# Performance work log

Hardware: AMD Instinct MI355X
Metric: run time of the kernel (lower is better)

Reference implementation:

```python
import jax, jax.numpy as jnp
import numpy as np

G, N, EPG = 32, 128, 2048   # graphs, nodes/graph (uniform), edges/graph
H, L = 128, 2               # hidden_dim, num_layers
OUT = 12


def setup_inputs() -> dict:
    key = jax.random.key(0)
    ks = jax.random.split(key, 32)
    x = jax.random.randint(ks[0], (G * N, 9), 0, 2, dtype=jnp.int32)
    edge_attr = jax.random.randint(ks[1], (G * EPG, 3), 0, 2, dtype=jnp.int32)
    # edges stay within their own graph (global ids = local + graph offset)
    src = jax.random.randint(ks[2], (G, EPG), 0, N, dtype=jnp.int32)
    dst = jax.random.randint(ks[3], (G, EPG), 0, N, dtype=jnp.int32)
    off = (jnp.arange(G, dtype=jnp.int32) * N)[:, None]
    edge_index = jnp.stack([(src + off).reshape(-1), (dst + off).reshape(-1)]).astype(jnp.int64)
    batch_idx = (jnp.arange(G * N) // N).astype(jnp.int32)

    def p(k, shape, scale=0.05):
        return jax.random.normal(k, shape, dtype=jnp.float32) * scale

    return dict(
        x=x, edge_index=edge_index, edge_attr=edge_attr, batch_idx=batch_idx,
        atom_tab=p(ks[4], (9, 119, H)), bond_tab=p(ks[5], (3, 8, H)),
        W_m1=p(ks[6], (L, 2 * H, H)), b_m1=jnp.zeros((L, H), jnp.float32),
        W_m2=p(ks[7], (L, 2 * H, H)), b_m2=jnp.zeros((L, H), jnp.float32),
        W_me=p(ks[8], (L, H, H)), b_me=jnp.zeros((L, H), jnp.float32),
        W_mg=p(ks[9], (L, H, H)), b_mg=jnp.zeros((L, H), jnp.float32),
        W_h1=p(ks[10], (L, H, H)), b_h1=jnp.zeros((L, H), jnp.float32),
        W_h2=p(ks[11], (L, H, H)), b_h2=jnp.zeros((L, H), jnp.float32),
        W_o1=p(ks[12], (L, 2 * H, H)), b_o1=jnp.zeros((L, H), jnp.float32),
        W_o2=p(ks[13], (L, H, H)), b_o2=jnp.zeros((L, H), jnp.float32),
        Wg1=p(ks[14], (H, H)), bg1=jnp.zeros((H,), jnp.float32),
        Wg2=p(ks[15], (H, OUT)), bg2=jnp.zeros((OUT,), jnp.float32),
    )


def reference(x, edge_index, edge_attr, batch_idx, atom_tab, bond_tab,
              W_m1, b_m1, W_m2, b_m2, W_me, b_me, W_mg, b_mg,
              W_h1, b_h1, W_h2, b_h2, W_o1, b_o1, W_o2, b_o2,
              Wg1, bg1, Wg2, bg2):
    # Atom/Bond encoders: sum of per-feature embeddings
    node_fts = jnp.sum(jax.vmap(lambda t, i: t[i], in_axes=(0, 1))(atom_tab, x), axis=0)        # (G*N, H)
    edge_fts = jnp.sum(jax.vmap(lambda t, i: t[i], in_axes=(0, 1))(bond_tab, edge_attr), axis=0)  # (E, H)

    # dense adjacency + dense edge features (one fused scatter, replaces per-graph loop)
    g = (edge_index[0] // N).astype(jnp.int32)
    s = (edge_index[0] % N).astype(jnp.int32)
    d = (edge_index[1] % N).astype(jnp.int32)
    adj = jnp.zeros((G, N, N), jnp.float32).at[g, s, d].set(1.0)
    edense = jnp.zeros((G, N, N, H), jnp.float32).at[g, s, d].set(edge_fts)

    nd = node_fts.reshape(G, N, H)          # to_dense_batch (uniform graphs -> no padding)
    gf = jnp.zeros((G, H), jnp.float32)
    hid = jnp.zeros_like(nd)
    NEG = jnp.float32(-1e9)

    for l in range(L):  # CLRS MPNN layers
        z = jnp.concatenate([nd, hid], axis=-1)                 # (G, N, 2H)
        m1 = z @ W_m1[l] + b_m1[l]
        m2 = z @ W_m2[l] + b_m2[l]
        me = edense @ W_me[l] + b_me[l]                         # (G, N, N, H)
        mg = gf @ W_mg[l] + b_mg[l]
        msgs = m1[:, None, :, :] + m2[:, :, None, :] + me + mg[:, None, None, :]
        h = jax.nn.relu(msgs)
        h = jax.nn.relu(h @ W_h1[l] + b_h1[l]) @ W_h2[l] + b_h2[l]
        h = jnp.where(adj[..., None] > 0, h, NEG)               # masked max over senders
        agg = jnp.max(h, axis=1)                                # (G, N, H)
        hid = jax.nn.relu(z @ W_o1[l] + b_o1[l] + agg @ W_o2[l] + b_o2[l])

    emb = hid.mean(axis=1)                                      # (G, H)
    return jax.nn.relu(emb @ Wg1 + bg1) @ Wg2 + bg2             # (G, OUT)
```

## Files before the change

kernel.cpp:

```cpp
#include <hip/hip_runtime.h>

#define Gg   32
#define Nn   128
#define Hh   128
#define Ee   65536
#define GN   4096
#define GNN  524288

typedef unsigned short ushort_t;
typedef __attribute__((ext_vector_type(8))) __bf16 bf16x8;
typedef __attribute__((ext_vector_type(4))) float f32x4;
struct us4 { ushort_t a, b, c, d; };

__device__ __forceinline__ float reluf(float x) { return x > 0.f ? x : 0.f; }

__device__ __forceinline__ unsigned fkey(float f) {
  unsigned u = __float_as_uint(f);
  return (u & 0x80000000u) ? ~u : (u | 0x80000000u);
}
__device__ __forceinline__ float funkey(unsigned k) {
  unsigned u = (k & 0x80000000u) ? (k ^ 0x80000000u) : ~k;
  return __uint_as_float(u);
}

__device__ __forceinline__ ushort_t bfh(float x) {
  unsigned u = __float_as_uint(x);
  return (ushort_t)((u + 0x7FFFu + ((u >> 16) & 1u)) >> 16);
}
__device__ __forceinline__ void split2(float x, ushort_t& h, ushort_t& l) {
  h = bfh(x);
  float hf = __uint_as_float(((unsigned)h) << 16);
  l = bfh(x - hf);
}

__global__ __launch_bounds__(256) void k_wprep_all(const float* __restrict__ W_h1,
                                                   const float* __restrict__ W_h2,
                                                   const float* __restrict__ W_o1,
                                                   const float* __restrict__ W_o2,
                                                   const float* __restrict__ W_m1,
                                                   const float* __restrict__ W_m2,
                                                   ushort_t* __restrict__ wt,
                                                   ushort_t* __restrict__ wo,
                                                   ushort_t* __restrict__ wm,
                                                   int* __restrict__ win,
                                                   int* __restrict__ cnt) {
  int b = blockIdx.x;
  int tid = threadIdx.x;
  if (b < 256) {
    int t = b * 256 + tid;
    int l = t >> 15;
    int m = (t >> 14) & 1;
    int e = t & 16383;
    int n = e & 127, k = e >> 7;
    const float* W = (m == 0 ? W_h1 : W_h2) + l * 16384;
    float v = W[k * 128 + n];
    ushort_t h, lo;
    split2(v, h, lo);
    int nf = n >> 4, lr = n & 15, kf = k >> 5, lg = (k >> 3) & 3, j = k & 7;
    int off = ((nf * 4 + kf) * 64 + lg * 16 + lr) * 8 + j;
    int base = ((l * 2 + m) * 2) * 16384;
    wt[base + off] = h;
    wt[base + 16384 + off] = lo;
  } else if (b < 640) {
    int ep = (b - 256) * 256 + tid;
    int l = (ep >= 49152) ? 1 : 0;
    int e = ep - l * 49152;
    int n = e / 384, k = e - n * 384;
    float v = (k < 256) ? W_o1[(l * 256 + k) * 128 + n]
                        : W_o2[(l * 128 + (k - 256)) * 128 + n];
    ushort_t h, lo;
    split2(v, h, lo);
    int nf = n >> 4, lr = n & 15, kf = k >> 5, lg = (k >> 3) & 3, j = k & 7;
    int off = ((nf * 12 + kf) * 64 + lg * 16 + lr) * 8 + j;
    wo[(l * 2 + 0) * 49152 + off] = h;
    wo[(l * 2 + 1) * 49152 + off] = lo;
  } else if (b < 1152) {
    int t = (b - 640) * 256 + tid;
    int l = t >> 16;
    int m = (t >> 15) & 1;
    int e = t & 32767;
    int n = e >> 8, k = e & 255;
    const float* W = (m == 0 ? W_m1 : W_m2);
    float v = W[(l * 256 + k) * 128 + n];
    ushort_t h, lo;
    split2(v, h, lo);
    int nf = n >> 4, lr = n & 15, kf = k >> 5, lg = (k >> 3) & 3, j = k & 7;
    int off = ((nf * 8 + kf) * 64 + lg * 16 + lr) * 8 + j;
    int base = ((l * 2 + m) * 2) * 32768;
    wm[base + off] = h;
    wm[base + 32768 + off] = lo;
  } else {
    int idx = (b - 1152) * 256 + tid;
    ((int4*)win)[idx] = make_int4(-1, -1, -1, -1);
    if (idx == 0) *cnt = 0;
  }
}

__global__ __launch_bounds__(256) void k_scatter_win(const int* __restrict__ e32,
                                                     int* __restrict__ win) {
  __shared__ int sflag;
  int tid = threadIdx.x;
  if (tid == 0) sflag = 0;
  __syncthreads();
  if (tid < 128 && e32[2 * tid + 1] != 0) atomicOr(&sflag, 1);
  __syncthreads();
  int e = blockIdx.x * 256 + tid;
  int sg, dg;
  if (sflag) { sg = e32[e]; dg = e32[Ee + e]; }
  else       { sg = e32[2 * e]; dg = e32[2 * Ee + 2 * e]; }
  int g = sg / Nn;
  int s = sg % Nn;
  int d = dg % Nn;
  atomicMax(&win[(g * Nn + d) * Nn + s], e);
}

__global__ __launch_bounds__(256) void k_dfill2(const int* __restrict__ win,
                                                const int* __restrict__ eattr,
                                                int* __restrict__ cnt,
                                                unsigned* __restrict__ recs) {
  int tid = threadIdx.x;
  int grp = tid >> 7, t = tid & 127;
  int dest = blockIdx.x * 2 + grp;
  int e = win[dest * 128 + t];
  bool valid = e >= 0;
  unsigned long long mask = __ballot(valid);
  __shared__ int cw[4];
  __shared__ int sbase;
  int lane = tid & 63, wv = tid >> 6;
  if (lane == 0) cw[wv] = __popcll(mask);
  __syncthreads();
  if (tid == 0) {
    int tot = cw[0] + cw[1] + cw[2] + cw[3];
    sbase = tot ? atomicAdd(cnt, tot) : 0;
  }
  __syncthreads();
  if (valid) {
    int off = __popcll(mask & ((1ull << lane) - 1));
    if (wv & 1) off += cw[grp * 2];
    if (grp) off += cw[0] + cw[1];
    int a0 = eattr[e * 3 + 0], a1 = eattr[e * 3 + 1], a2 = eattr[e * 3 + 2];
    unsigned code = (unsigned)(a0 + (a1 << 3) + (a2 << 6));
    unsigned idx = ((unsigned)dest << 7) | (unsigned)t;
    recs[sbase + off] = (idx << 9) | code;
  }
}

__global__ __launch_bounds__(256) void k_me2(const float* __restrict__ bond_tab,
                                             const float* __restrict__ W_me,
                                             const float* __restrict__ b_me,
                                             const float* __restrict__ b_mg,
                                             float* __restrict__ me0,
                                             float* __restrict__ me1,
                                             unsigned* __restrict__ aggkA,
                                             unsigned* __restrict__ aggkB) {
  int bx = blockIdx.x;
  int l = bx >> 8, b2 = bx & 255;
  const float* W = W_me + l * 16384;
  const float* bme = b_me + l * 128;
  const float* bmg = b_mg + l * 128;
  float* me = l ? me1 : me0;
  unsigned* aggk = l ? aggkB : aggkA;
  __shared__ float v[2][128];
  int tid = threadIdx.x;
  int half = tid >> 7, j = tid & 127;
  int c = b2 * 2 + half;
  int a0 = c & 7, a1 = (c >> 3) & 7, a2 = (c >> 6) & 7;
  v[half][j] = bond_tab[a0 * 128 + j] + bond_tab[(8 + a1) * 128 + j] +
               bond_tab[(16 + a2) * 128 + j];
  __syncthreads();
  float acc = bme[j] + bmg[j];
  for (int i = 0; i < 128; ++i) acc += v[half][i] * W[i * 128 + j];
  me[c * 128 + j] = acc;
  unsigned key = fkey(-1.0e9f);
#pragma unroll
  for (int i = 0; i < 8; ++i) aggk[b2 * 2048 + i * 256 + tid] = key;
}

__device__ __forceinline__ void load_afrag(const ushort_t (*MH)[136],
                                           const ushort_t (*ML)[136],
                                           int row, int lg,
                                           bf16x8 ah[4], bf16x8 al[4]) {
#pragma unroll
  for (int kf = 0; kf < 4; ++kf) {
    ah[kf] = *(const bf16x8*)&MH[row][lg * 8 + 32 * kf];
    al[kf] = *(const bf16x8*)&ML[row][lg * 8 + 32 * kf];
  }
}

__device__ __forceinline__ void load_afrag264(const ushort_t (*MH)[264],
                                              const ushort_t (*ML)[264],
                                              int row, int base, int lg,
                                              bf16x8 ah[4], bf16x8 al[4]) {
#pragma unroll
  for (int kf = 0; kf < 4; ++kf) {
    ah[kf] = *(const bf16x8*)&MH[row][base + lg * 8 + 32 * kf];
    al[kf] = *(const bf16x8*)&ML[row][base + lg * 8 + 32 * kf];
  }
}

__global__ __launch_bounds__(256) void k_encode_m12(const int* __restrict__ x,
                                                    const float* __restrict__ atom_tab,
                                                    const ushort_t* __restrict__ wm,
                                                    const float* __restrict__ bi1,
                                                    const float* __restrict__ bi2,
                                                    float* __restrict__ nf_,
                                                    float* __restrict__ hid,
                                                    float* __restrict__ m1,
                                                    float* __restrict__ m2) {
  __shared__ ushort_t AH[16][136];
  __shared__ ushort_t AL[16][136];
  __shared__ int xs[144];
  int tid = threadIdx.x;
  int v0 = blockIdx.x * 16;
  if (tid < 144) xs[tid] = x[v0 * 9 + tid];
  __syncthreads();
#pragma unroll
  for (int i = 0; i < 8; ++i) {
    int e = tid + i * 256;
    int row = e >> 7, col = e & 127;
    float s = 0.f;
#pragma unroll
    for (int f = 0; f < 9; ++f) {
      int idx = xs[row * 9 + f];
      s += atom_tab[(f * 119 + idx) * Hh + col];
    }
    nf_[(v0 + row) * Hh + col] = s;
    hid[(v0 + row) * Hh + col] = 0.f;
    ushort_t h, l;
    split2(s, h, l);
    AH[row][col] = h;
    AL[row][col] = l;
  }
  __syncthreads();
  int lane = tid & 63, wid = tid >> 6;
  int lr = lane & 15, lg = lane >> 4;
  f32x4 a1[2], a2[2];
#pragma unroll
  for (int i = 0; i < 2; ++i) { a1[i] = (f32x4){0.f,0.f,0.f,0.f}; a2[i] = (f32x4){0.f,0.f,0.f,0.f}; }
  const ushort_t* w1h = wm;
  const ushort_t* w1l = wm + 32768;
  const ushort_t* w2h = wm + 65536;
  const ushort_t* w2l = wm + 98304;
  bf16x8 ah[4], al[4];
  load_afrag(AH, AL, lr, lg, ah, al);
#pragma unroll
  for (int jj = 0; jj < 2; ++jj) {
    int nfr = 2 * wid + jj;
#pragma unroll
    for (int kf = 0; kf < 4; ++kf) {
      int ch = ((nfr * 8 + kf) << 9) + lane * 8;
      bf16x8 b1h = *(const bf16x8*)(w1h + ch);
      bf16x8 b1l = *(const bf16x8*)(w1l + ch);
      bf16x8 b2h = *(const bf16x8*)(w2h + ch);
      bf16x8 b2l = *(const bf16x8*)(w2l + ch);
      a1[jj] = __builtin_amdgcn_mfma_f32_16x16x32_bf16(ah[kf], b1h, a1[jj], 0, 0, 0);
      a1[jj] = __builtin_amdgcn_mfma_f32_16x16x32_bf16(ah[kf], b1l, a1[jj], 0, 0, 0);
      a1[jj] = __builtin_amdgcn_mfma_f32_16x16x32_bf16(al[kf], b1h, a1[jj], 0, 0, 0);
      a2[jj] = __builtin_amdgcn_mfma_f32_16x16x32_bf16(ah[kf], b2h, a2[jj], 0, 0, 0);
      a2[jj] = __builtin_amdgcn_mfma_f32_16x16x32_bf16(ah[kf], b2l, a2[jj], 0, 0, 0);
      a2[jj] = __builtin_amdgcn_mfma_f32_16x16x32_bf16(al[kf], b2h, a2[jj], 0, 0, 0);
    }
  }
#pragma unroll
  for (int jj = 0; jj < 2; ++jj) {
    int col = 16 * (2 * wid + jj) + lr;
    float bb1 = bi1[col], bb2 = bi2[col];
#pragma unroll
    for (int reg = 0; reg < 4; ++reg) {
      int row = v0 + lg * 4 + reg;
      m1[row * Hh + col] = a1[jj][reg] + bb1;
      m2[row * Hh + col] = a2[jj][reg] + bb2;
    }
  }
}

__global__ __launch_bounds__(512) void k_edge(const unsigned* __restrict__ recs,
                                              const int* __restrict__ cnt,
                                              const float* __restrict__ m1,
                                              const float* __restrict__ m2,
                                              const float* __restrict__ me,
                                              const ushort_t* __restrict__ wt1h,
                                              const ushort_t* __restrict__ wt1l,
                                              const ushort_t* __restrict__ wt2h,
                                              const ushort_t* __restrict__ wt2l,
                                              const float* __restrict__ b_h1,
                                              const float* __restrict__ b_h2,
                                              unsigned* __restrict__ aggk) {
  __shared__ ushort_t MH[64][136];
  __shared__ ushort_t ML[64][136];
  __shared__ unsigned srec[64];
  int tid = threadIdx.x;
  int n = *cnt;
  if (tid < 64) {
    int r = blockIdx.x * 64 + tid;
    srec[tid] = (r < n) ? recs[r] : 0xFFFFFFFFu;
  }
  __syncthreads();
  {
    int c4 = tid & 31, rq = tid >> 5;
#pragma unroll
    for (int i = 0; i < 4; ++i) {
      int r = 16 * i + rq;
      float4 v = make_float4(0.f, 0.f, 0.f, 0.f);
      unsigned rec = srec[r];
      if (rec != 0xFFFFFFFFu) {
        int code = rec & 511;
        unsigned idx = rec >> 9;
        int s = idx & 127, d = (idx >> 7) & 127, g = idx >> 14;
        float4 a = *(const float4*)(m1 + (((g << 7) + d) << 7) + c4 * 4);
        float4 b = *(const float4*)(m2 + (((g << 7) + s) << 7) + c4 * 4);
        float4 cme = *(const float4*)(me + (code << 7) + c4 * 4);
        v.x = reluf(a.x + b.x + cme.x);
        v.y = reluf(a.y + b.y + cme.y);
        v.z = reluf(a.z + b.z + cme.z);
        v.w = reluf(a.w + b.w + cme.w);
      }
      us4 h4, l4;
      split2(v.x, h4.a, l4.a); split2(v.y, h4.b, l4.b);
      split2(v.z, h4.c, l4.c); split2(v.w, h4.d, l4.d);
      *(us4*)&MH[r][c4 * 4] = h4;
      *(us4*)&ML[r][c4 * 4] = l4;
    }
  }
  __syncthreads();

  int lane = tid & 63, wid = tid >> 6;
  int lr = lane & 15, lg = lane >> 4;
  float b1v = b_h1[16 * wid + lr];
  float b2v = b_h2[16 * wid + lr];
  f32x4 acc[4];
#pragma unroll
  for (int rg = 0; rg < 4; ++rg) acc[rg] = (f32x4){0.f, 0.f, 0.f, 0.f};
#pragma unroll
  for (int rg = 0; rg < 4; ++rg) {
    bf16x8 ah[4], al[4];
    load_afrag(MH, ML, 16 * rg + lr, lg, ah, al);
#pragma unroll
    for (int kf = 0; kf < 4; ++kf) {
      int ch = ((wid * 4 + kf) << 9) + lane * 8;
      bf16x8 bh = *(const bf16x8*)(wt1h + ch);
      bf16x8 bl = *(const bf16x8*)(wt1l + ch);
      acc[rg] = __builtin_amdgcn_mfma_f32_16x16x32_bf16(ah[kf], bh, acc[rg], 0, 0, 0);
      acc[rg] = __builtin_amdgcn_mfma_f32_16x16x32_bf16(ah[kf], bl, acc[rg], 0, 0, 0);
      acc[rg] = __builtin_amdgcn_mfma_f32_16x16x32_bf16(al[kf], bh, acc[rg], 0, 0, 0);
    }
  }
  __syncthreads();
#pragma unroll
  for (int rg = 0; rg < 4; ++rg)
#pragma unroll
    for (int reg = 0; reg < 4; ++reg) {
      float t = reluf(acc[rg][reg] + b1v);
      int row = 16 * rg + lg * 4 + reg;
      int col = 16 * wid + lr;
      ushort_t h, l;
      split2(t, h, l);
      MH[row][col] = h;
      ML[row][col] = l;
    }
  __syncthreads();
#pragma unroll
  for (int rg = 0; rg < 4; ++rg) acc[rg] = (f32x4){0.f, 0.f, 0.f, 0.f};
#pragma unroll
  for (int rg = 0; rg < 4; ++rg) {
    bf16x8 ah[4], al[4];
    load_afrag(MH, ML, 16 * rg + lr, lg, ah, al);
#pragma unroll
    for (int kf = 0; kf < 4; ++kf) {
      int ch = ((wid * 4 + kf) << 9) + lane * 8;
      bf16x8 bh = *(const bf16x8*)(wt2h + ch);
      bf16x8 bl = *(const bf16x8*)(wt2l + ch);
      acc[rg] = __builtin_amdgcn_mfma_f32_16x16x32_bf16(ah[kf], bh, acc[rg], 0, 0, 0);
      acc[rg] = __builtin_amdgcn_mfma_f32_16x16x32_bf16(ah[kf], bl, acc[rg], 0, 0, 0);
      acc[rg] = __builtin_amdgcn_mfma_f32_16x16x32_bf16(al[kf], bh, acc[rg], 0, 0, 0);
    }
  }
  __syncthreads();
#pragma unroll
  for (int rg = 0; rg < 4; ++rg)
#pragma unroll
    for (int reg = 0; reg < 4; ++reg) {
      int row = 16 * rg + lg * 4 + reg;
      int col = 16 * wid + lr;
      unsigned b = __float_as_uint(acc[rg][reg] + b2v);
      MH[row][col] = (ushort_t)(b >> 16);
      ML[row][col] = (ushort_t)(b & 0xFFFFu);
    }
  __syncthreads();
  {
    int c = tid & 127, quarter = tid >> 7;
    int rbeg = quarter * 16, rend = rbeg + 16;
    unsigned curkey = 0xFFFFu;
    float best = -3.0e38f;
    for (int r = rbeg; r < rend; ++r) {
      unsigned rec = srec[r];
      unsigned key = rec >> 16;
      if (key != curkey) {
        if (curkey != 0xFFFFu)
          atomicMax(aggk + (curkey << 7) + c, fkey(best));
        curkey = key;
        best = -3.0e38f;
      }
      if (key != 0xFFFFu) {
        unsigned b = ((unsigned)MH[r][c] << 16) | (unsigned)ML[r][c];
        best = fmaxf(best, __uint_as_float(b));
      }
    }
    if (curkey != 0xFFFFu)
      atomicMax(aggk + (curkey << 7) + c, fkey(best));
  }
}

__global__ __launch_bounds__(256) void k_out(const float* __restrict__ nf,
                                             const float* __restrict__ hid,
                                             const unsigned* __restrict__ aggk,
                                             const ushort_t* __restrict__ wo_h,
                                             const ushort_t* __restrict__ wo_l,
                                             const float* __restrict__ bo1,
                                             const float* __restrict__ bo2,
                                             float* __restrict__ hidn) {
  __shared__ ushort_t MH[16][136];
  __shared__ ushort_t ML[16][136];
  int tid = threadIdx.x;
  int v0 = blockIdx.x * 16;
  int lane = tid & 63, wid = tid >> 6;
  int lr = lane & 15, lg = lane >> 4;
  f32x4 acc[2];
#pragma unroll
  for (int jj = 0; jj < 2; ++jj) acc[jj] = (f32x4){0.f, 0.f, 0.f, 0.f};

  for (int seg = 0; seg < 3; ++seg) {
#pragma unroll
    for (int i = 0; i < 2; ++i) {
      int idx = tid + i * 256;
      int row = idx >> 5, c4 = idx & 31;
      float4 v;
      if (seg == 0)      v = ((const float4*)nf)[(v0 + row) * 32 + c4];
      else if (seg == 1) v = ((const float4*)hid)[(v0 + row) * 32 + c4];
      else {
        uint4 k4 = ((const uint4*)aggk)[(v0 + row) * 32 + c4];
        v.x = funkey(k4.x); v.y = funkey(k4.y); v.z = funkey(k4.z); v.w = funkey(k4.w);
      }
      us4 h4, l4;
      split2(v.x, h4.a, l4.a);
      split2(v.y, h4.b, l4.b);
      split2(v.z, h4.c, l4.c);
      split2(v.w, h4.d, l4.d);
      *(us4*)&MH[row][c4 * 4] = h4;
      *(us4*)&ML[row][c4 * 4] = l4;
    }
    __syncthreads();
    bf16x8 ah[4], al[4];
    load_afrag(MH, ML, lr, lg, ah, al);
#pragma unroll
    for (int jj = 0; jj < 2; ++jj) {
      int nfr = 2 * wid + jj;
#pragma unroll
      for (int kf = 0; kf < 4; ++kf) {
        int ch = ((nfr * 12 + seg * 4 + kf) << 9) + lane * 8;
        bf16x8 bh = *(const bf16x8*)(wo_h + ch);
        bf16x8 bl = *(const bf16x8*)(wo_l + ch);
        acc[jj] = __builtin_amdgcn_mfma_f32_16x16x32_bf16(ah[kf], bh, acc[jj], 0, 0, 0);
        acc[jj] = __builtin_amdgcn_mfma_f32_16x16x32_bf16(ah[kf], bl, acc[jj], 0, 0, 0);
        acc[jj] = __builtin_amdgcn_mfma_f32_16x16x32_bf16(al[kf], bh, acc[jj], 0, 0, 0);
      }
    }
    __syncthreads();
  }
#pragma unroll
  for (int jj = 0; jj < 2; ++jj) {
    int col = 16 * (2 * wid + jj) + lr;
    float b = bo1[col] + bo2[col];
#pragma unroll
    for (int reg = 0; reg < 4; ++reg)
      hidn[(v0 + lg * 4 + reg) * Hh + col] = reluf(acc[jj][reg] + b);
  }
}

__global__ __launch_bounds__(256) void k_out_m12(const float* __restrict__ nf,
                                                 const float* __restrict__ hid,
                                                 const unsigned* __restrict__ aggk,
                                                 const ushort_t* __restrict__ wo_h,
                                                 const ushort_t* __restrict__ wo_l,
                                                 const float* __restrict__ bo1,
                                                 const float* __restrict__ bo2,
                                                 const ushort_t* __restrict__ wm,
                                                 const float* __restrict__ bm1,
                                                 const float* __restrict__ bm2,
                                                 float* __restrict__ hidn,
                                                 float* __restrict__ m1,
                                                 float* __restrict__ m2) {
  __shared__ ushort_t AH[16][264];
  __shared__ ushort_t AL[16][264];
  int tid = threadIdx.x;
  int v0 = blockIdx.x * 16;
  int lane = tid & 63, wid = tid >> 6;
  int lr = lane & 15, lg = lane >> 4;
  f32x4 acc[2];
#pragma unroll
  for (int jj = 0; jj < 2; ++jj) acc[jj] = (f32x4){0.f, 0.f, 0.f, 0.f};

  for (int seg = 0; seg < 3; ++seg) {
#pragma unroll
    for (int i = 0; i < 2; ++i) {
      int idx = tid + i * 256;
      int row = idx >> 5, c4 = idx & 31;
      float4 v;
      if (seg == 0)      v = ((const float4*)nf)[(v0 + row) * 32 + c4];
      else if (seg == 1) v = ((const float4*)hid)[(v0 + row) * 32 + c4];
      else {
        uint4 k4 = ((const uint4*)aggk)[(v0 + row) * 32 + c4];
        v.x = funkey(k4.x); v.y = funkey(k4.y); v.z = funkey(k4.z); v.w = funkey(k4.w);
      }
      us4 h4, l4;
      split2(v.x, h4.a, l4.a);
      split2(v.y, h4.b, l4.b);
      split2(v.z, h4.c, l4.c);
      split2(v.w, h4.d, l4.d);
      *(us4*)&AH[row][c4 * 4] = h4;
      *(us4*)&AL[row][c4 * 4] = l4;
    }
    __syncthreads();
    bf16x8 ah[4], al[4];
    load_afrag264(AH, AL, lr, 0, lg, ah, al);
#pragma unroll
    for (int jj = 0; jj < 2; ++jj) {
      int nfr = 2 * wid + jj;
#pragma unroll
      for (int kf = 0; kf < 4; ++kf) {
        int ch = ((nfr * 12 + seg * 4 + kf) << 9) + lane * 8;
        bf16x8 bh = *(const bf16x8*)(wo_h + ch);
        bf16x8 bl = *(const bf16x8*)(wo_l + ch);
        acc[jj] = __builtin_amdgcn_mfma_f32_16x16x32_bf16(ah[kf], bh, acc[jj], 0, 0, 0);
        acc[jj] = __builtin_amdgcn_mfma_f32_16x16x32_bf16(ah[kf], bl, acc[jj], 0, 0, 0);
        acc[jj] = __builtin_amdgcn_mfma_f32_16x16x32_bf16(al[kf], bh, acc[jj], 0, 0, 0);
      }
    }
    __syncthreads();
  }
#pragma unroll
  for (int jj = 0; jj < 2; ++jj) {
    int col = 16 * (2 * wid + jj) + lr;
    float b = bo1[col] + bo2[col];
#pragma unroll
    for (int reg = 0; reg < 4; ++reg) {
      float hv = reluf(acc[jj][reg] + b);
      int row = lg * 4 + reg;
      hidn[(v0 + row) * Hh + col] = hv;
      ushort_t h, l;
      split2(hv, h, l);
      AH[row][128 + col] = h;
      AL[row][128 + col] = l;
    }
  }
#pragma unroll
  for (int i = 0; i < 2; ++i) {
    int idx = tid + i * 256;
    int row = idx >> 5, c4 = idx & 31;
    float4 v = ((const float4*)nf)[(v0 + row) * 32 + c4];
    us4 h4, l4;
    split2(v.x, h4.a, l4.a);
    split2(v.y, h4.b, l4.b);
    split2(v.z, h4.c, l4.c);
    split2(v.w, h4.d, l4.d);
    *(us4*)&AH[row][c4 * 4] = h4;
    *(us4*)&AL[row][c4 * 4] = l4;
  }
  __syncthreads();
  f32x4 a1[2], a2[2];
#pragma unroll
  for (int i = 0; i < 2; ++i) { a1[i] = (f32x4){0.f,0.f,0.f,0.f}; a2[i] = (f32x4){0.f,0.f,0.f,0.f}; }
  const ushort_t* w1h = wm;
  const ushort_t* w1l = wm + 32768;
  const ushort_t* w2h = wm + 65536;
  const ushort_t* w2l = wm + 98304;
#pragma unroll
  for (int seg = 0; seg < 2; ++seg) {
    bf16x8 ah[4], al[4];
    load_afrag264(AH, AL, lr, seg * 128, lg, ah, al);
#pragma unroll
    for (int jj = 0; jj < 2; ++jj) {
      int nfr = 2 * wid + jj;
#pragma unroll
      for (int kf = 0; kf < 4; ++kf) {
        int ch = ((nfr * 8 + seg * 4 + kf) << 9) + lane * 8;
        bf16x8 b1h = *(const bf16x8*)(w1h + ch);
        bf16x8 b1l = *(const bf16x8*)(w1l + ch);
        bf16x8 b2h = *(const bf16x8*)(w2h + ch);
        bf16x8 b2l = *(const bf16x8*)(w2l + ch);
        a1[jj] = __builtin_amdgcn_mfma_f32_16x16x32_bf16(ah[kf], b1h, a1[jj], 0, 0, 0);
        a1[jj] = __builtin_amdgcn_mfma_f32_16x16x32_bf16(ah[kf], b1l, a1[jj], 0, 0, 0);
        a1[jj] = __builtin_amdgcn_mfma_f32_16x16x32_bf16(al[kf], b1h, a1[jj], 0, 0, 0);
        a2[jj] = __builtin_amdgcn_mfma_f32_16x16x32_bf16(ah[kf], b2h, a2[jj], 0, 0, 0);
        a2[jj] = __builtin_amdgcn_mfma_f32_16x16x32_bf16(ah[kf], b2l, a2[jj], 0, 0, 0);
        a2[jj] = __builtin_amdgcn_mfma_f32_16x16x32_bf16(al[kf], b2h, a2[jj], 0, 0, 0);
      }
    }
  }
#pragma unroll
  for (int jj = 0; jj < 2; ++jj) {
    int col = 16 * (2 * wid + jj) + lr;
    float bb1 = bm1[col], bb2 = bm2[col];
#pragma unroll
    for (int reg = 0; reg < 4; ++reg) {
      int row = v0 + lg * 4 + reg;
      m1[row * Hh + col] = a1[jj][reg] + bb1;
      m2[row * Hh + col] = a2[jj][reg] + bb2;
    }
  }
}

__global__ __launch_bounds__(128) void k_head(const float* __restrict__ hid,
                                              const float* __restrict__ Wg1,
                                              const float* __restrict__ bg1,
                                              const float* __restrict__ Wg2,
                                              const float* __restrict__ bg2,
                                              float* __restrict__ out) {
  __shared__ float emb[Hh];
  __shared__ float tt[Hh];
  int g = blockIdx.x, j = threadIdx.x;
  float s = 0.f;
  for (int n = 0; n < Nn; ++n) s += hid[(g * Nn + n) * Hh + j];
  emb[j] = s * (1.f / Nn);
  __syncthreads();
  float a = bg1[j];
  for (int i = 0; i < Hh; ++i) a += emb[i] * Wg1[i * Hh + j];
  tt[j] = reluf(a);
  __syncthreads();
  if (j < 12) {
    float o = bg2[j];
    for (int i = 0; i < Hh; ++i) o += tt[i] * Wg2[i * 12 + j];
    out[g * 12 + j] = o;
  }
}

extern "C" void kernel_launch(void* const* d_in, const int* in_sizes, int n_in,
                              void* d_out, int out_size, void* d_ws, size_t ws_size,
                              hipStream_t stream) {
  const int* x = (const int*)d_in[0];
  const int* eidx32 = (const int*)d_in[1];
  const int* eattr = (const int*)d_in[2];
  const float* atom_tab = (const float*)d_in[4];
  const float* bond_tab = (const float*)d_in[5];
  const float* W_m1 = (const float*)d_in[6];
  const float* b_m1 = (const float*)d_in[7];
  const float* W_m2 = (const float*)d_in[8];
  const float* b_m2 = (const float*)d_in[9];
  const float* W_me = (const float*)d_in[10];
  const float* b_me = (const float*)d_in[11];
  const float* b_mg = (const float*)d_in[13];
  const float* W_h1 = (const float*)d_in[14];
  const float* b_h1 = (const float*)d_in[15];
  const float* W_h2 = (const float*)d_in[16];
  const float* b_h2 = (const float*)d_in[17];
  const float* W_o1 = (const float*)d_in[18];
  const float* b_o1 = (const float*)d_in[19];
  const float* W_o2 = (const float*)d_in[20];
  const float* b_o2 = (const float*)d_in[21];
  const float* Wg1 = (const float*)d_in[22];
  const float* bg1 = (const float*)d_in[23];
  const float* Wg2 = (const float*)d_in[24];
  const float* bg2 = (const float*)d_in[25];
  float* out = (float*)d_out;

  char* ws = (char*)d_ws;
  float* nf = (float*)(ws);
  float* hidA = (float*)(ws + (2u << 20));
  float* hidB = (float*)(ws + (4u << 20));
  float* m1 = (float*)(ws + (6u << 20));
  float* m2 = (float*)(ws + (8u << 20));
  unsigned* aggkA = (unsigned*)(ws + (10u << 20));
  int* win = (int*)(ws + (12u << 20));
  ushort_t* wt = (ushort_t*)(ws + (14u << 20));
  float* me0 = (float*)(ws + (14u << 20) + (256u << 10));
  float* me1 = (float*)(ws + (14u << 20) + (512u << 10));
  unsigned* recs = (unsigned*)(ws + (15u << 20));
  int* cnt = (int*)(ws + (15u << 20) + (256u << 10));
  unsigned* aggkB = (unsigned*)(ws + (16u << 20));
  ushort_t* wo = (ushort_t*)(ws + (18u << 20));
  ushort_t* wm = (ushort_t*)(ws + (18u << 20) + (512u << 10));

  k_wprep_all<<<1664, 256, 0, stream>>>(W_h1, W_h2, W_o1, W_o2, W_m1, W_m2,
                                        wt, wo, wm, win, cnt);
  k_me2<<<512, 256, 0, stream>>>(bond_tab, W_me, b_me, b_mg, me0, me1, aggkA, aggkB);
  k_encode_m12<<<256, 256, 0, stream>>>(x, atom_tab, wm, b_m1, b_m2,
                                        nf, hidA, m1, m2);
  k_scatter_win<<<256, 256, 0, stream>>>(eidx32, win);
  k_dfill2<<<2048, 256, 0, stream>>>(win, eattr, cnt, recs);

  k_edge<<<1024, 512, 0, stream>>>(recs, cnt, m1, m2, me0,
                                   wt + 0 * 16384, wt + 1 * 16384,
                                   wt + 2 * 16384, wt + 3 * 16384,
                                   b_h1, b_h2, aggkA);
  k_out_m12<<<256, 256, 0, stream>>>(nf, hidA, aggkA,
                                     wo + 0 * 49152, wo + 1 * 49152,
                                     b_o1, b_o2,
                                     wm + 131072, b_m1 + Hh, b_m2 + Hh,
                                     hidB, m1, m2);
  k_edge<<<1024, 512, 0, stream>>>(recs, cnt, m1, m2, me1,
                                   wt + 4 * 16384, wt + 5 * 16384,
                                   wt + 6 * 16384, wt + 7 * 16384,
                                   b_h1 + Hh, b_h2 + Hh, aggkB);
  k_out<<<256, 256, 0, stream>>>(nf, hidB, aggkB,
                                 wo + 2 * 49152, wo + 3 * 49152,
                                 b_o1 + Hh, b_o2 + Hh, hidA);
  k_head<<<32, 128, 0, stream>>>(hidA, Wg1, bg1, Wg2, bg2, out);
}
```

Before: 134.5 us.

## Build destination-sorted edge records via count, scan, and fill instead of atomic append

Replaces the single fill kernel that appended each block's valid edges at an atomic counter with three kernels: per-destination counts, a single-block exclusive scan producing a row pointer array, and a fill that writes each destination's records at its scanned offset. The records become deterministically ordered by destination (CSR-like), which should give the edge kernels better locality and less contention on the max-aggregation keys. The cost is two extra kernel launches and a serial single-block scan on the critical path.

```diff
diff --git a/kernel.cpp b/kernel.cpp
--- a/kernel.cpp
+++ b/kernel.cpp
@@ -42,8 +42,7 @@
                                                    ushort_t* __restrict__ wt,
                                                    ushort_t* __restrict__ wo,
                                                    ushort_t* __restrict__ wm,
-                                                   int* __restrict__ win,
-                                                   int* __restrict__ cnt) {
+                                                   int* __restrict__ win) {
   int b = blockIdx.x;
   int tid = threadIdx.x;
   if (b < 256) {
@@ -92,7 +91,6 @@
   } else {
     int idx = (b - 1152) * 256 + tid;
     ((int4*)win)[idx] = make_int4(-1, -1, -1, -1);
-    if (idx == 0) *cnt = 0;
   }
 }
 
@@ -114,10 +112,58 @@
   atomicMax(&win[(g * Nn + d) * Nn + s], e);
 }
 
-__global__ __launch_bounds__(256) void k_dfill2(const int* __restrict__ win,
-                                                const int* __restrict__ eattr,
-                                                int* __restrict__ cnt,
-                                                unsigned* __restrict__ recs) {
+__global__ __launch_bounds__(256) void k_dcount(const int* __restrict__ win,
+                                                int* __restrict__ dcnt) {
+  int tid = threadIdx.x;
+  int grp = tid >> 7, t = tid & 127;
+  int dest = blockIdx.x * 2 + grp;
+  bool valid = win[dest * 128 + t] >= 0;
+  unsigned long long mask = __ballot(valid);
+  __shared__ int cw[4];
+  if ((tid & 63) == 0) cw[tid >> 6] = __popcll(mask);
+  __syncthreads();
+  if (t == 0) dcnt[dest] = cw[grp * 2] + cw[grp * 2 + 1];
+}
+
+__global__ __launch_bounds__(512) void k_dscan(const int* __restrict__ dcnt,
+                                               int* __restrict__ rowptr) {
+  int tid = threadIdx.x;
+  int c0, c1, c2, c3, c4, c5, c6, c7;
+  int bi = tid * 8;
+  c0 = dcnt[bi + 0]; c1 = dcnt[bi + 1]; c2 = dcnt[bi + 2]; c3 = dcnt[bi + 3];
+  c4 = dcnt[bi + 4]; c5 = dcnt[bi + 5]; c6 = dcnt[bi + 6]; c7 = dcnt[bi + 7];
+  int s = c0 + c1 + c2 + c3 + c4 + c5 + c6 + c7;
+  int x = s;
+#pragma unroll
+  for (int off = 1; off < 64; off <<= 1) {
+    int y = __shfl_up(x, off, 64);
+    if ((tid & 63) >= off) x += y;
+  }
+  __shared__ int wsum[8], woff[8];
+  if ((tid & 63) == 63) wsum[tid >> 6] = x;
+  __syncthreads();
+  if (tid == 0) {
+    int a = 0;
+#pragma unroll
+    for (int i = 0; i < 8; ++i) { woff[i] = a; a += wsum[i]; }
+  }
+  __syncthreads();
+  int base = x - s + woff[tid >> 6];
+  rowptr[bi + 0] = base; base += c0;
+  rowptr[bi + 1] = base; base += c1;
+  rowptr[bi + 2] = base; base += c2;
+  rowptr[bi + 3] = base; base += c3;
+  rowptr[bi + 4] = base; base += c4;
+  rowptr[bi + 5] = base; base += c5;
+  rowptr[bi + 6] = base; base += c6;
+  rowptr[bi + 7] = base; base += c7;
+  if (tid == 511) rowptr[4096] = base;
+}
+
+__global__ __launch_bounds__(256) void k_dfill(const int* __restrict__ win,
+                                               const int* __restrict__ eattr,
+                                               const int* __restrict__ rowptr,
+                                               unsigned* __restrict__ recs) {
   int tid = threadIdx.x;
   int grp = tid >> 7, t = tid & 127;
   int dest = blockIdx.x * 2 + grp;
@@ -125,23 +171,16 @@
   bool valid = e >= 0;
   unsigned long long mask = __ballot(valid);
   __shared__ int cw[4];
-  __shared__ int sbase;
-  int lane = tid & 63, wv = tid >> 6;
-  if (lane == 0) cw[wv] = __popcll(mask);
-  __syncthreads();
-  if (tid == 0) {
-    int tot = cw[0] + cw[1] + cw[2] + cw[3];
-    sbase = tot ? atomicAdd(cnt, tot) : 0;
-  }
+  int lane = tid & 63;
+  if (lane == 0) cw[tid >> 6] = __popcll(mask);
   __syncthreads();
   if (valid) {
     int off = __popcll(mask & ((1ull << lane) - 1));
-    if (wv & 1) off += cw[grp * 2];
-    if (grp) off += cw[0] + cw[1];
+    if ((tid >> 6) & 1) off += cw[grp * 2];
     int a0 = eattr[e * 3 + 0], a1 = eattr[e * 3 + 1], a2 = eattr[e * 3 + 2];
     unsigned code = (unsigned)(a0 + (a1 << 3) + (a2 << 6));
     unsigned idx = ((unsigned)dest << 7) | (unsigned)t;
-    recs[sbase + off] = (idx << 9) | code;
+    recs[rowptr[dest] + off] = (idx << 9) | code;
   }
 }
 
@@ -675,18 +714,23 @@
   float* me0 = (float*)(ws + (14u << 20) + (256u << 10));
   float* me1 = (float*)(ws + (14u << 20) + (512u << 10));
   unsigned* recs = (unsigned*)(ws + (15u << 20));
-  int* cnt = (int*)(ws + (15u << 20) + (256u << 10));
+  int* dcnt = (int*)(ws + (15u << 20) + (256u << 10));
+  int* rowptr = (int*)(ws + (15u << 20) + (272u << 10));
   unsigned* aggkB = (unsigned*)(ws + (16u << 20));
   ushort_t* wo = (ushort_t*)(ws + (18u << 20));
   ushort_t* wm = (ushort_t*)(ws + (18u << 20) + (512u << 10));
 
   k_wprep_all<<<1664, 256, 0, stream>>>(W_h1, W_h2, W_o1, W_o2, W_m1, W_m2,
-                                        wt, wo, wm, win, cnt);
+                                        wt, wo, wm, win);
   k_me2<<<512, 256, 0, stream>>>(bond_tab, W_me, b_me, b_mg, me0, me1, aggkA, aggkB);
   k_encode_m12<<<256, 256, 0, stream>>>(x, atom_tab, wm, b_m1, b_m2,
                                         nf, hidA, m1, m2);
   k_scatter_win<<<256, 256, 0, stream>>>(eidx32, win);
-  k_dfill2<<<2048, 256, 0, stream>>>(win, eattr, cnt, recs);
+  k_dcount<<<2048, 256, 0, stream>>>(win, dcnt);
+  k_dscan<<<1, 512, 0, stream>>>(dcnt, rowptr);
+  k_dfill<<<2048, 256, 0, stream>>>(win, eattr, rowptr, recs);
+
+  int* cnt = rowptr + 4096;
 
   k_edge<<<1024, 512, 0, stream>>>(recs, cnt, m1, m2, me0,
                                    wt + 0 * 16384, wt + 1 * 16384,
```

After: 115.9 us. 1.16x faster.
